# Performance work log

Measured on AMD Instinct MI355X. Metric: run time of the kernel, lower is better.

Reference implementation:

```python
import jax, jax.numpy as jnp
import numpy as np

N_NODES = 200000
N_EDGES = 600000
IN_CH = 128
OUT_CH = 128
E_DIM = 16


def _linear_params(key, fan_in, fan_out):
    kw, kb = jax.random.split(key)
    s = 1.0 / np.sqrt(fan_in)
    W = jax.random.uniform(kw, (fan_in, fan_out), jnp.float32, -s, s)
    b = jax.random.uniform(kb, (fan_out,), jnp.float32, -s, s)
    return W, b


def setup_inputs() -> dict:
    key = jax.random.key(0)
    ks = jax.random.split(key, 12)
    x = jax.random.normal(ks[0], (N_NODES, IN_CH), jnp.float32)
    edge_index = jax.random.randint(ks[1], (2, N_EDGES), 0, N_NODES, jnp.int64)
    edge_attr = jax.random.normal(ks[2], (N_EDGES, E_DIM), jnp.float32)
    W_enc, b_enc = _linear_params(ks[3], IN_CH, OUT_CH)
    # conv1: edge lin (e_dim->out) + 2-layer MLP, trainable eps (init 0)
    We1, be1 = _linear_params(ks[4], E_DIM, OUT_CH)
    W11, b11 = _linear_params(ks[5], OUT_CH, OUT_CH)
    W12, b12 = _linear_params(ks[6], OUT_CH, OUT_CH)
    eps1 = jnp.zeros((), jnp.float32)
    # conv2
    We2, be2 = _linear_params(ks[7], E_DIM, OUT_CH)
    W21, b21 = _linear_params(ks[8], OUT_CH, OUT_CH)
    W22, b22 = _linear_params(ks[9], OUT_CH, OUT_CH)
    eps2 = jnp.zeros((), jnp.float32)
    return {"x": x, "edge_index": edge_index, "edge_attr": edge_attr,
            "W_enc": W_enc, "b_enc": b_enc,
            "We1": We1, "be1": be1, "W11": W11, "b11": b11, "W12": W12, "b12": b12, "eps1": eps1,
            "We2": We2, "be2": be2, "W21": W21, "b21": b21, "W22": W22, "b22": b22, "eps2": eps2}


def _gine_conv(h, src, dst, edge_feat, eps, W1, b1, W2, b2):
    # message: ReLU(x_j + lin_edge(edge_attr)); aggregate: scatter-sum to dst
    msg = jax.nn.relu(h[src] + edge_feat)          # [E, C]
    agg = jax.ops.segment_sum(msg, dst, num_segments=h.shape[0])  # [N, C]
    z = (1.0 + eps) * h + agg
    z = jax.nn.relu(z @ W1 + b1)
    return jax.nn.relu(z @ W2 + b2)


def reference(x, edge_index, edge_attr,
              W_enc, b_enc,
              We1, be1, W11, b11, W12, b12, eps1,
              We2, be2, W21, b21, W22, b22, eps2):
    src, dst = edge_index[0], edge_index[1]
    h = jax.nn.relu(x @ W_enc + b_enc)
    ef1 = edge_attr @ We1 + be1
    h = jax.nn.relu(_gine_conv(h, src, dst, ef1, eps1, W11, b11, W12, b12))
    # dropout (p=0.2) is identity in eval mode
    ef2 = edge_attr @ We2 + be2
    out = jax.nn.relu(_gine_conv(h, src, dst, ef2, eps2, W21, b21, W22, b22))
    return out
```

## Files before the change

kernel.cpp:

```cpp
#include <hip/hip_runtime.h>
#include <stdint.h>

#define N_NODES 200000
#define N_EDGES 600000
#define SCAN_CHUNK 1024
#define SCAN_BLOCKS ((N_NODES + SCAN_CHUNK - 1) / SCAN_CHUNK)
#define GRID_AGG 4096
#define NWAVES (GRID_AGG * 4)

typedef __attribute__((ext_vector_type(8))) short short8;
typedef __attribute__((ext_vector_type(4))) float floatx4;
typedef __attribute__((ext_vector_type(2))) float floatx2;

static __device__ __forceinline__ unsigned short f2bf(float f) {
  union { float f; unsigned u; } c; c.f = f;
  unsigned u = c.u;
  unsigned r = (u + 0x7fffu + ((u >> 16) & 1u)) >> 16;
  return (unsigned short)r;
}
static __device__ __forceinline__ float asf(unsigned u) {
  union { unsigned u; float f; } c; c.u = u; return c.f;
}

__global__ __launch_bounds__(256) void prep_kernel(
    const float* w0, const float* w1, const float* w2, const float* w3, const float* w4,
    unsigned short* out) {
  const float* src;
  switch (blockIdx.y) {
    case 0: src = w0; break;
    case 1: src = w1; break;
    case 2: src = w2; break;
    case 3: src = w3; break;
    default: src = w4; break;
  }
  unsigned short* dst = out + (size_t)blockIdx.y * 16384;
  int t = blockIdx.x * 256 + threadIdx.x;
#pragma unroll
  for (int i = 0; i < 4; ++i) {
    int idx = t + 4096 * i;
    int n = idx >> 7, k = idx & 127;
    dst[idx] = f2bf(src[k * 128 + n]);
  }
}

__global__ __launch_bounds__(256) void hist_kernel(const int* __restrict__ dst, int* deg, int E) {
  int e = blockIdx.x * 256 + threadIdx.x;
  if (e < E) atomicAdd(&deg[dst[e]], 1);
}

__global__ __launch_bounds__(256) void scan_sum_kernel(const int* __restrict__ deg, int* partial,
                                                       int n) {
  __shared__ int wsum[4];
  const int tid = threadIdx.x, lane = tid & 63, wid = tid >> 6;
  int idx0 = blockIdx.x * SCAN_CHUNK + tid * 4;
  int s = 0;
#pragma unroll
  for (int j = 0; j < 4; ++j) {
    int ix = idx0 + j;
    if (ix < n) s += deg[ix];
  }
#pragma unroll
  for (int d = 32; d >= 1; d >>= 1) s += __shfl_down(s, d, 64);
  if (lane == 0) wsum[wid] = s;
  __syncthreads();
  if (tid == 0) partial[blockIdx.x] = wsum[0] + wsum[1] + wsum[2] + wsum[3];
}

__global__ __launch_bounds__(256) void scan_partials_kernel(int* partial, int* off, int nb, int n) {
  __shared__ int wsum[4];
  const int tid = threadIdx.x, lane = tid & 63, wid = tid >> 6;
  int val = (tid < nb) ? partial[tid] : 0;
  int incl = val;
#pragma unroll
  for (int d = 1; d < 64; d <<= 1) {
    int t = __shfl_up(incl, d, 64);
    if (lane >= d) incl += t;
  }
  if (lane == 63) wsum[wid] = incl;
  __syncthreads();
  int base = 0;
  for (int w = 0; w < wid; ++w) base += wsum[w];
  int excl = base + incl - val;
  if (tid < nb) partial[tid] = excl;
  if (tid == 0) off[n] = wsum[0] + wsum[1] + wsum[2] + wsum[3];
}

__global__ __launch_bounds__(256) void scan_apply_kernel(const int* __restrict__ partial, int* off,
                                                         int* cursor, int n) {
  __shared__ int wsum[4];
  const int tid = threadIdx.x, lane = tid & 63, wid = tid >> 6;
  int idx0 = blockIdx.x * SCAN_CHUNK + tid * 4;
  int v[4];
  int s = 0;
#pragma unroll
  for (int j = 0; j < 4; ++j) {
    int ix = idx0 + j;
    v[j] = (ix < n) ? off[ix] : 0;
    s += v[j];
  }
  int incl = s;
#pragma unroll
  for (int d = 1; d < 64; d <<= 1) {
    int t = __shfl_up(incl, d, 64);
    if (lane >= d) incl += t;
  }
  if (lane == 63) wsum[wid] = incl;
  __syncthreads();
  int base = partial[blockIdx.x];
  for (int w = 0; w < wid; ++w) base += wsum[w];
  int running = base + incl - s;
#pragma unroll
  for (int j = 0; j < 4; ++j) {
    int ix = idx0 + j;
    if (ix < n) { off[ix] = running; cursor[ix] = running; }
    running += v[j];
  }
}

__global__ __launch_bounds__(256) void scatter_kernel(const int* __restrict__ dst,
                                                      const int* __restrict__ src,
                                                      const float* __restrict__ eattr, int* cursor,
                                                      int* srcs, float* eaC, int E) {
  int e = blockIdx.x * 256 + threadIdx.x;
  if (e < E) {
    int p = atomicAdd(&cursor[dst[e]], 1);
    srcs[p] = src[e];
    const float4* q = (const float4*)(eattr + (size_t)e * 16);
    float4* o = (float4*)(eaC + (size_t)p * 16);
    o[0] = q[0]; o[1] = q[1]; o[2] = q[2]; o[3] = q[3];
  }
}

__global__ __launch_bounds__(256) void partition_kernel(const int* __restrict__ off,
                                                        int* waveStart) {
  int w = blockIdx.x * 256 + threadIdx.x;
  if (w > NWAVES) return;
  if (w == NWAVES) { waveStart[w] = N_NODES; return; }
  long long t = (long long)w * N_EDGES / NWAVES;
  int lo = 0, hi = N_NODES;
  while (lo < hi) {
    int mid = (lo + hi) >> 1;
    if (off[mid] < (int)t) lo = mid + 1; else hi = mid;
  }
  waveStart[w] = lo;
}

__global__ __launch_bounds__(256) void agg_z_kernel(
    const unsigned short* __restrict__ hB, const int* __restrict__ off,
    const int* __restrict__ waveStart, const int* __restrict__ srcs,
    const float* __restrict__ eaC,
    const float* __restrict__ We, const float* __restrict__ be,
    const float* __restrict__ epsPtr, unsigned short* __restrict__ z) {
  const int lane = threadIdx.x & 63;
  const int wv = threadIdx.x >> 6;
  const int c = lane * 2;
  floatx2 wr[16];
#pragma unroll
  for (int d = 0; d < 16; ++d) {
    float2 t = *((const float2*)(We + d * 128 + c));
    wr[d].x = t.x; wr[d].y = t.y;
  }
  const float2 bev = *((const float2*)(be + c));
  const float epsp = 1.0f + epsPtr[0];
  const int w = blockIdx.x * 4 + wv;
  const int n0 = waveStart[w];
  const int n1 = waveStart[w + 1];
  if (n0 >= n1) return;

  int obase = n0;
  {
    int ix = obase + lane; if (ix > n1) ix = n1;
  }
  int ix0 = obase + lane; if (ix0 > n1) ix0 = n1;
  int offv = off[ix0];
  int ii = __builtin_amdgcn_readlane(offv, 0);
  int ebase = ii;
  int sx0 = ebase + lane; if (sx0 > N_EDGES - 1) sx0 = N_EDGES - 1;
  int sbuf = srcs[sx0];

#define EDGE_COMPUTE(EIDX, HW) { \
    const float* ea = eaC + (size_t)(EIDX) * 16; \
    const float4 q0 = *((const float4*)(ea)); \
    const float4 q1 = *((const float4*)(ea + 4)); \
    const float4 q2 = *((const float4*)(ea + 8)); \
    const float4 q3 = *((const float4*)(ea + 12)); \
    floatx2 efa; efa.x = bev.x; efa.y = bev.y; \
    floatx2 efb; efb.x = 0.0f; efb.y = 0.0f; \
    efa += q0.x * wr[0]; efb += q0.y * wr[1]; \
    efa += q0.z * wr[2]; efb += q0.w * wr[3]; \
    efa += q1.x * wr[4]; efb += q1.y * wr[5]; \
    efa += q1.z * wr[6]; efb += q1.w * wr[7]; \
    efa += q2.x * wr[8]; efb += q2.y * wr[9]; \
    efa += q2.z * wr[10]; efb += q2.w * wr[11]; \
    efa += q3.x * wr[12]; efb += q3.y * wr[13]; \
    efa += q3.z * wr[14]; efb += q3.w * wr[15]; \
    floatx2 hv; hv.x = asf((HW) << 16); hv.y = asf((HW) & 0xffff0000u); \
    floatx2 mm = (efa + efb) + hv; \
    mm.x = fmaxf(mm.x, 0.0f); mm.y = fmaxf(mm.y, 0.0f); \
    acc += mm; }

  for (int n = n0; n < n1; ++n) {
    if (n + 1 - obase >= 64) {
      obase = n;
      int ix = obase + lane; if (ix > n1) ix = n1;
      offv = off[ix];
    }
    const int eE = __builtin_amdgcn_readlane(offv, n + 1 - obase);
    const unsigned hwn = *((const unsigned*)(hB + (size_t)n * 128 + c));
    floatx2 acc; acc.x = 0.0f; acc.y = 0.0f;
    while (ii < eE) {
      int m = eE - ii; if (m > 4) m = 4;
      if (ii + m > ebase + 64) {
        ebase = ii;
        int sx = ebase + lane; if (sx > N_EDGES - 1) sx = N_EDGES - 1;
        sbuf = srcs[sx];
      }
      const int j = ii - ebase;
      const int sn0 = __builtin_amdgcn_readlane(sbuf, j);
      const int sn1_ = __builtin_amdgcn_readlane(sbuf, (j + 1) & 63);
      const int sn2_ = __builtin_amdgcn_readlane(sbuf, (j + 2) & 63);
      const int sn3_ = __builtin_amdgcn_readlane(sbuf, (j + 3) & 63);
      unsigned hw0, hw1 = 0, hw2 = 0, hw3 = 0;
      hw0 = *((const unsigned*)(hB + (size_t)sn0 * 128 + c));
      if (m > 1) hw1 = *((const unsigned*)(hB + (size_t)sn1_ * 128 + c));
      if (m > 2) hw2 = *((const unsigned*)(hB + (size_t)sn2_ * 128 + c));
      if (m > 3) hw3 = *((const unsigned*)(hB + (size_t)sn3_ * 128 + c));
      EDGE_COMPUTE(ii, hw0);
      if (m > 1) EDGE_COMPUTE(ii + 1, hw1);
      if (m > 2) EDGE_COMPUTE(ii + 2, hw2);
      if (m > 3) EDGE_COMPUTE(ii + 3, hw3);
      ii += m;
    }
    const float hx = asf(hwn << 16);
    const float hy = asf(hwn & 0xffff0000u);
    unsigned p = (unsigned)f2bf(fmaf(epsp, hx, acc.x)) |
                 ((unsigned)f2bf(fmaf(epsp, hy, acc.y)) << 16);
    *((unsigned*)(z + (size_t)n * 128 + c)) = p;
  }
#undef EDGE_COMPUTE
}

__global__ __launch_bounds__(256) void mlp_kernel(
    const void* __restrict__ Ain, int aIsBf16,
    const unsigned short* __restrict__ W1t, const float* __restrict__ b1,
    const unsigned short* __restrict__ W2t, const float* __restrict__ b2,
    int twoStage, int outBf16, void* __restrict__ out) {
  __shared__ unsigned short sA[64][136];
  __shared__ unsigned short sW[128][136];
  const int tid = threadIdx.x;
  const int lane = tid & 63;
  const int wv = tid >> 6;
  const int lr = lane & 15, quad = lane >> 4;
  const int mw = wv >> 1, nw = wv & 1;
  const size_t rowBase = (size_t)blockIdx.x * 64;

  if (aIsBf16) {
    const uint4* src = (const uint4*)((const unsigned short*)Ain + rowBase * 128);
#pragma unroll
    for (int i = 0; i < 4; ++i) {
      int idx = tid + 256 * i;
      int r = idx >> 4, c8 = idx & 15;
      uint4 v = src[idx];
      *((uint4*)&sA[r][c8 * 8]) = v;
    }
  } else {
    const float4* src = (const float4*)((const float*)Ain + rowBase * 128);
#pragma unroll
    for (int i = 0; i < 8; ++i) {
      int idx = tid + 256 * i;
      int r = idx >> 5, c4 = idx & 31;
      float4 v = src[idx];
      uint2 p;
      p.x = (unsigned)f2bf(v.x) | ((unsigned)f2bf(v.y) << 16);
      p.y = (unsigned)f2bf(v.z) | ((unsigned)f2bf(v.w) << 16);
      *((uint2*)&sA[r][c4 * 4]) = p;
    }
  }
  {
    const uint4* srcw = (const uint4*)W1t;
#pragma unroll
    for (int i = 0; i < 8; ++i) {
      int idx = tid + 256 * i;
      int r = idx >> 4, c8 = idx & 15;
      *((uint4*)&sW[r][c8 * 8]) = srcw[idx];
    }
  }
  __syncthreads();

  floatx4 acc[2][4];
#pragma unroll
  for (int mi = 0; mi < 2; ++mi)
#pragma unroll
    for (int ni = 0; ni < 4; ++ni)
#pragma unroll
      for (int i = 0; i < 4; ++i) acc[mi][ni][i] = 0.0f;

#pragma unroll
  for (int kk = 0; kk < 4; ++kk) {
    short8 a[2], b[4];
#pragma unroll
    for (int mi = 0; mi < 2; ++mi)
      a[mi] = *((const short8*)&sA[32 * mw + 16 * mi + lr][kk * 32 + quad * 8]);
#pragma unroll
    for (int ni = 0; ni < 4; ++ni)
      b[ni] = *((const short8*)&sW[64 * nw + 16 * ni + lr][kk * 32 + quad * 8]);
#pragma unroll
    for (int mi = 0; mi < 2; ++mi)
#pragma unroll
      for (int ni = 0; ni < 4; ++ni)
        acc[mi][ni] = __builtin_amdgcn_mfma_f32_16x16x32_bf16(a[mi], b[ni], acc[mi][ni], 0, 0, 0);
  }

  if (!twoStage) {
#pragma unroll
    for (int mi = 0; mi < 2; ++mi)
#pragma unroll
      for (int ni = 0; ni < 4; ++ni)
#pragma unroll
        for (int i = 0; i < 4; ++i) {
          int row = 32 * mw + 16 * mi + quad * 4 + i;
          int col = 64 * nw + 16 * ni + lr;
          float v = fmaxf(acc[mi][ni][i] + b1[col], 0.0f);
          if (outBf16)
            ((unsigned short*)out)[(rowBase + row) * 128 + col] = f2bf(v);
          else
            ((float*)out)[(rowBase + row) * 128 + col] = v;
        }
    return;
  }

  __syncthreads();
#pragma unroll
  for (int mi = 0; mi < 2; ++mi)
#pragma unroll
    for (int ni = 0; ni < 4; ++ni)
#pragma unroll
      for (int i = 0; i < 4; ++i) {
        int row = 32 * mw + 16 * mi + quad * 4 + i;
        int col = 64 * nw + 16 * ni + lr;
        sA[row][col] = f2bf(fmaxf(acc[mi][ni][i] + b1[col], 0.0f));
      }
  {
    const uint4* srcw = (const uint4*)W2t;
#pragma unroll
    for (int i = 0; i < 8; ++i) {
      int idx = tid + 256 * i;
      int r = idx >> 4, c8 = idx & 15;
      *((uint4*)&sW[r][c8 * 8]) = srcw[idx];
    }
  }
  __syncthreads();

  floatx4 acc2[2][4];
#pragma unroll
  for (int mi = 0; mi < 2; ++mi)
#pragma unroll
    for (int ni = 0; ni < 4; ++ni)
#pragma unroll
      for (int i = 0; i < 4; ++i) acc2[mi][ni][i] = 0.0f;

#pragma unroll
  for (int kk = 0; kk < 4; ++kk) {
    short8 a[2], b[4];
#pragma unroll
    for (int mi = 0; mi < 2; ++mi)
      a[mi] = *((const short8*)&sA[32 * mw + 16 * mi + lr][kk * 32 + quad * 8]);
#pragma unroll
    for (int ni = 0; ni < 4; ++ni)
      b[ni] = *((const short8*)&sW[64 * nw + 16 * ni + lr][kk * 32 + quad * 8]);
#pragma unroll
    for (int mi = 0; mi < 2; ++mi)
#pragma unroll
      for (int ni = 0; ni < 4; ++ni)
        acc2[mi][ni] = __builtin_amdgcn_mfma_f32_16x16x32_bf16(a[mi], b[ni], acc2[mi][ni], 0, 0, 0);
  }

#pragma unroll
  for (int mi = 0; mi < 2; ++mi)
#pragma unroll
    for (int ni = 0; ni < 4; ++ni)
#pragma unroll
      for (int i = 0; i < 4; ++i) {
        int row = 32 * mw + 16 * mi + quad * 4 + i;
        int col = 64 * nw + 16 * ni + lr;
        float v = fmaxf(acc2[mi][ni][i] + b2[col], 0.0f);
        if (outBf16)
          ((unsigned short*)out)[(rowBase + row) * 128 + col] = f2bf(v);
        else
          ((float*)out)[(rowBase + row) * 128 + col] = v;
      }
}

extern "C" void kernel_launch(void* const* d_in, const int* in_sizes, int n_in,
                              void* d_out, int out_size, void* d_ws, size_t ws_size,
                              hipStream_t stream) {
  (void)in_sizes; (void)n_in; (void)out_size; (void)ws_size;
  const float* x = (const float*)d_in[0];
  const int* eidx = (const int*)d_in[1];
  const int* esrc = eidx;
  const int* edst = eidx + N_EDGES;
  const float* eattr = (const float*)d_in[2];
  const float* W_enc = (const float*)d_in[3];
  const float* b_enc = (const float*)d_in[4];
  const float* We1 = (const float*)d_in[5];
  const float* be1 = (const float*)d_in[6];
  const float* W11 = (const float*)d_in[7];
  const float* b11 = (const float*)d_in[8];
  const float* W12 = (const float*)d_in[9];
  const float* b12 = (const float*)d_in[10];
  const float* eps1 = (const float*)d_in[11];
  const float* We2 = (const float*)d_in[12];
  const float* be2 = (const float*)d_in[13];
  const float* W21 = (const float*)d_in[14];
  const float* b21 = (const float*)d_in[15];
  const float* W22 = (const float*)d_in[16];
  const float* b22 = (const float*)d_in[17];
  const float* eps2 = (const float*)d_in[18];

  char* ws = (char*)d_ws;
  size_t o = 0;
  unsigned short* wt = (unsigned short*)(ws + o); o += 163840;
  unsigned short* hB = (unsigned short*)(ws + o); o += 51200000ull;
  unsigned short* bufZ = (unsigned short*)(ws + o); o += 51200000ull;
  float* eaC = (float*)(ws + o); o += 38400000ull;
  int* off = (int*)(ws + o); o += ((N_NODES + 1) * 4 + 15) / 16 * 16;
  int* cursor = (int*)(ws + o); o += ((size_t)N_NODES * 4 + 15) / 16 * 16;
  int* srcs = (int*)(ws + o); o += (size_t)N_EDGES * 4;
  int* partial = (int*)(ws + o); o += (SCAN_BLOCKS * 4 + 15) / 16 * 16;
  int* waveStart = (int*)(ws + o); o += (size_t)(NWAVES + 1) * 4;

  unsigned short* Wt_enc = wt;
  unsigned short* Wt11 = wt + 16384;
  unsigned short* Wt12 = wt + 2 * 16384;
  unsigned short* Wt21 = wt + 3 * 16384;
  unsigned short* Wt22 = wt + 4 * 16384;

  hipMemsetAsync(off, 0, (N_NODES + 1) * sizeof(int), stream);
  prep_kernel<<<dim3(16, 5), 256, 0, stream>>>(W_enc, W11, W12, W21, W22, wt);

  mlp_kernel<<<3125, 256, 0, stream>>>(x, 0, Wt_enc, b_enc, Wt_enc, b_enc, 0, 1, hB);

  hist_kernel<<<(N_EDGES + 255) / 256, 256, 0, stream>>>(edst, off, N_EDGES);
  scan_sum_kernel<<<SCAN_BLOCKS, 256, 0, stream>>>(off, partial, N_NODES);
  scan_partials_kernel<<<1, 256, 0, stream>>>(partial, off, SCAN_BLOCKS, N_NODES);
  scan_apply_kernel<<<SCAN_BLOCKS, 256, 0, stream>>>(partial, off, cursor, N_NODES);
  partition_kernel<<<(NWAVES + 256) / 256, 256, 0, stream>>>(off, waveStart);
  scatter_kernel<<<(N_EDGES + 255) / 256, 256, 0, stream>>>(edst, esrc, eattr, cursor, srcs, eaC,
                                                            N_EDGES);

  agg_z_kernel<<<GRID_AGG, 256, 0, stream>>>(hB, off, waveStart, srcs, eaC, We1, be1, eps1, bufZ);
  mlp_kernel<<<3125, 256, 0, stream>>>(bufZ, 1, Wt11, b11, Wt12, b12, 1, 1, hB);
  agg_z_kernel<<<GRID_AGG, 256, 0, stream>>>(hB, off, waveStart, srcs, eaC, We2, be2, eps2, bufZ);
  mlp_kernel<<<3125, 256, 0, stream>>>(bufZ, 1, Wt21, b21, Wt22, b22, 1, 0, d_out);
}
```

Measured before the change: 515.6 us.

## Restructure edge aggregation into flat edge stream with 8-wide gather batches

The per-node loop with inner edge batches of up to 4 is replaced by a single loop over the wave's contiguous edge range. Each step gathers up to 8 source rows at once, and the node boundaries are handled by flushing the accumulator whenever the edge index reaches the next offset. Batches no longer stop at node boundaries, which is meant to raise memory-level parallelism for low-degree nodes. The packed float2 math is split into scalar FMAs, with asm barriers to keep the weights in VGPRs. The cost is higher register pressure and more complex control flow inside the unrolled loop.

```diff
diff --git a/kernel.cpp b/kernel.cpp
--- a/kernel.cpp
+++ b/kernel.cpp
@@ -10,7 +10,6 @@
 
 typedef __attribute__((ext_vector_type(8))) short short8;
 typedef __attribute__((ext_vector_type(4))) float floatx4;
-typedef __attribute__((ext_vector_type(2))) float floatx2;
 
 static __device__ __forceinline__ unsigned short f2bf(float f) {
   union { float f; unsigned u; } c; c.f = f;
@@ -154,11 +153,16 @@
   const int lane = threadIdx.x & 63;
   const int wv = threadIdx.x >> 6;
   const int c = lane * 2;
-  floatx2 wr[16];
+  float wx[16], wy[16];
 #pragma unroll
   for (int d = 0; d < 16; ++d) {
     float2 t = *((const float2*)(We + d * 128 + c));
-    wr[d].x = t.x; wr[d].y = t.y;
+    wx[d] = t.x; wy[d] = t.y;
+  }
+#pragma unroll
+  for (int d = 0; d < 16; ++d) {
+    asm volatile("" : "+v"(wx[d]));
+    asm volatile("" : "+v"(wy[d]));
   }
   const float2 bev = *((const float2*)(be + c));
   const float epsp = 1.0f + epsPtr[0];
@@ -168,15 +172,29 @@
   if (n0 >= n1) return;
 
   int obase = n0;
-  {
-    int ix = obase + lane; if (ix > n1) ix = n1;
-  }
-  int ix0 = obase + lane; if (ix0 > n1) ix0 = n1;
-  int offv = off[ix0];
-  int ii = __builtin_amdgcn_readlane(offv, 0);
-  int ebase = ii;
-  int sx0 = ebase + lane; if (sx0 > N_EDGES - 1) sx0 = N_EDGES - 1;
-  int sbuf = srcs[sx0];
+  int ox = obase + lane; if (ox > N_NODES) ox = N_NODES;
+  int offv = off[ox];
+  int n = n0;
+  int e = __builtin_amdgcn_readlane(offv, 0);
+  int eE = __builtin_amdgcn_readlane(offv, 1);
+  const int eTot = off[n1];
+  unsigned hwn = *((const unsigned*)(hB + (size_t)n * 128 + c));
+
+  int ebase = e;
+  int sx = ebase + lane; if (sx > N_EDGES - 1) sx = N_EDGES - 1;
+  int sbuf = srcs[sx];
+
+  float accx = 0.0f, accy = 0.0f;
+
+#define FLUSH() do { \
+    const float hx = asf(hwn << 16); \
+    const float hy = asf(hwn & 0xffff0000u); \
+    unsigned p = (unsigned)f2bf(fmaf(epsp, hx, accx)) | \
+                 ((unsigned)f2bf(fmaf(epsp, hy, accy)) << 16); \
+    *((unsigned*)(z + (size_t)n * 128 + c)) = p; \
+    accx = 0.0f; accy = 0.0f; \
+    ++n; \
+  } while (0)
 
 #define EDGE_COMPUTE(EIDX, HW) { \
     const float* ea = eaC + (size_t)(EIDX) * 16; \
@@ -184,60 +202,67 @@
     const float4 q1 = *((const float4*)(ea + 4)); \
     const float4 q2 = *((const float4*)(ea + 8)); \
     const float4 q3 = *((const float4*)(ea + 12)); \
-    floatx2 efa; efa.x = bev.x; efa.y = bev.y; \
-    floatx2 efb; efb.x = 0.0f; efb.y = 0.0f; \
-    efa += q0.x * wr[0]; efb += q0.y * wr[1]; \
-    efa += q0.z * wr[2]; efb += q0.w * wr[3]; \
-    efa += q1.x * wr[4]; efb += q1.y * wr[5]; \
-    efa += q1.z * wr[6]; efb += q1.w * wr[7]; \
-    efa += q2.x * wr[8]; efb += q2.y * wr[9]; \
-    efa += q2.z * wr[10]; efb += q2.w * wr[11]; \
-    efa += q3.x * wr[12]; efb += q3.y * wr[13]; \
-    efa += q3.z * wr[14]; efb += q3.w * wr[15]; \
-    floatx2 hv; hv.x = asf((HW) << 16); hv.y = asf((HW) & 0xffff0000u); \
-    floatx2 mm = (efa + efb) + hv; \
-    mm.x = fmaxf(mm.x, 0.0f); mm.y = fmaxf(mm.y, 0.0f); \
-    acc += mm; }
-
-  for (int n = n0; n < n1; ++n) {
-    if (n + 1 - obase >= 64) {
-      obase = n;
-      int ix = obase + lane; if (ix > n1) ix = n1;
-      offv = off[ix];
-    }
-    const int eE = __builtin_amdgcn_readlane(offv, n + 1 - obase);
-    const unsigned hwn = *((const unsigned*)(hB + (size_t)n * 128 + c));
-    floatx2 acc; acc.x = 0.0f; acc.y = 0.0f;
-    while (ii < eE) {
-      int m = eE - ii; if (m > 4) m = 4;
-      if (ii + m > ebase + 64) {
-        ebase = ii;
-        int sx = ebase + lane; if (sx > N_EDGES - 1) sx = N_EDGES - 1;
-        sbuf = srcs[sx];
+    float ax = bev.x, bx = 0.0f, ay = bev.y, by = 0.0f; \
+    ax = fmaf(q0.x, wx[0], ax); ay = fmaf(q0.x, wy[0], ay); \
+    bx = fmaf(q0.y, wx[1], bx); by = fmaf(q0.y, wy[1], by); \
+    ax = fmaf(q0.z, wx[2], ax); ay = fmaf(q0.z, wy[2], ay); \
+    bx = fmaf(q0.w, wx[3], bx); by = fmaf(q0.w, wy[3], by); \
+    ax = fmaf(q1.x, wx[4], ax); ay = fmaf(q1.x, wy[4], ay); \
+    bx = fmaf(q1.y, wx[5], bx); by = fmaf(q1.y, wy[5], by); \
+    ax = fmaf(q1.z, wx[6], ax); ay = fmaf(q1.z, wy[6], ay); \
+    bx = fmaf(q1.w, wx[7], bx); by = fmaf(q1.w, wy[7], by); \
+    ax = fmaf(q2.x, wx[8], ax); ay = fmaf(q2.x, wy[8], ay); \
+    bx = fmaf(q2.y, wx[9], bx); by = fmaf(q2.y, wy[9], by); \
+    ax = fmaf(q2.z, wx[10], ax); ay = fmaf(q2.z, wy[10], ay); \
+    bx = fmaf(q2.w, wx[11], bx); by = fmaf(q2.w, wy[11], by); \
+    ax = fmaf(q3.x, wx[12], ax); ay = fmaf(q3.x, wy[12], ay); \
+    bx = fmaf(q3.y, wx[13], bx); by = fmaf(q3.y, wy[13], by); \
+    ax = fmaf(q3.z, wx[14], ax); ay = fmaf(q3.z, wy[14], ay); \
+    bx = fmaf(q3.w, wx[15], bx); by = fmaf(q3.w, wy[15], by); \
+    float mx = (ax + bx) + asf((HW) << 16); \
+    float my = (ay + by) + asf((HW) & 0xffff0000u); \
+    accx += fmaxf(mx, 0.0f); \
+    accy += fmaxf(my, 0.0f); }
+
+  while (e < eTot) {
+    int m = eTot - e; if (m > 8) m = 8;
+    if (e + m > ebase + 64) {
+      ebase = e;
+      int s2 = ebase + lane; if (s2 > N_EDGES - 1) s2 = N_EDGES - 1;
+      sbuf = srcs[s2];
+    }
+    const int j = e - ebase;
+    unsigned hw[8];
+#pragma unroll
+    for (int k = 0; k < 8; ++k) {
+      if (k < m) {
+        const int sn = __builtin_amdgcn_readlane(sbuf, j + k);
+        hw[k] = *((const unsigned*)(hB + (size_t)sn * 128 + c));
       }
-      const int j = ii - ebase;
-      const int sn0 = __builtin_amdgcn_readlane(sbuf, j);
-      const int sn1_ = __builtin_amdgcn_readlane(sbuf, (j + 1) & 63);
-      const int sn2_ = __builtin_amdgcn_readlane(sbuf, (j + 2) & 63);
-      const int sn3_ = __builtin_amdgcn_readlane(sbuf, (j + 3) & 63);
-      unsigned hw0, hw1 = 0, hw2 = 0, hw3 = 0;
-      hw0 = *((const unsigned*)(hB + (size_t)sn0 * 128 + c));
-      if (m > 1) hw1 = *((const unsigned*)(hB + (size_t)sn1_ * 128 + c));
-      if (m > 2) hw2 = *((const unsigned*)(hB + (size_t)sn2_ * 128 + c));
-      if (m > 3) hw3 = *((const unsigned*)(hB + (size_t)sn3_ * 128 + c));
-      EDGE_COMPUTE(ii, hw0);
-      if (m > 1) EDGE_COMPUTE(ii + 1, hw1);
-      if (m > 2) EDGE_COMPUTE(ii + 2, hw2);
-      if (m > 3) EDGE_COMPUTE(ii + 3, hw3);
-      ii += m;
-    }
-    const float hx = asf(hwn << 16);
-    const float hy = asf(hwn & 0xffff0000u);
-    unsigned p = (unsigned)f2bf(fmaf(epsp, hx, acc.x)) |
-                 ((unsigned)f2bf(fmaf(epsp, hy, acc.y)) << 16);
-    *((unsigned*)(z + (size_t)n * 128 + c)) = p;
+    }
+#pragma unroll
+    for (int k = 0; k < 8; ++k) {
+      if (k >= m) break;
+      while (e == eE) {
+        FLUSH();
+        if (n + 1 - obase >= 64) {
+          obase = n;
+          int ox2 = obase + lane; if (ox2 > N_NODES) ox2 = N_NODES;
+          offv = off[ox2];
+        }
+        eE = __builtin_amdgcn_readlane(offv, n + 1 - obase);
+        hwn = *((const unsigned*)(hB + (size_t)n * 128 + c));
+      }
+      EDGE_COMPUTE(e, hw[k]);
+      ++e;
+    }
+  }
+  while (n < n1) {
+    FLUSH();
+    if (n < n1) hwn = *((const unsigned*)(hB + (size_t)n * 128 + c));
   }
 #undef EDGE_COMPUTE
+#undef FLUSH
 }
 
 __global__ __launch_bounds__(256) void mlp_kernel(
```

After: 653.1 us. +26.7%, slower.
